# Kernel optimization log

Measured on AMD Instinct MI355X. Metric: run time of the kernel, lower is better.

Reference implementation:

```python
import jax, jax.numpy as jnp
import numpy as np

NUM_HEADS = 16
GROUP_NUM = 4
HIDDEN = 1024
HEAD_DIM = HIDDEN // NUM_HEADS
EPS = 1e-5


def layernorm(x, g, b):
    mu = jnp.mean(x, axis=-1, keepdims=True)
    var = jnp.var(x, axis=-1, keepdims=True)
    return (x - mu) * jax.lax.rsqrt(var + EPS) * g + b


def setup_inputs() -> dict:
    key = jax.random.key(0)
    ks = jax.random.split(key, 12)
    s = 0.02
    return {
        "hidden_state": jax.random.normal(ks[0], (2, 2048, HIDDEN), jnp.float32),
        "wq": jax.random.normal(ks[1], (HIDDEN, HIDDEN), jnp.float32) * s,
        "bq": jnp.zeros((HIDDEN,), jnp.float32),
        "wk": jax.random.normal(ks[2], (GROUP_NUM * HEAD_DIM, HIDDEN), jnp.float32) * s,
        "bk": jnp.zeros((GROUP_NUM * HEAD_DIM,), jnp.float32),
        "wv": jax.random.normal(ks[3], (GROUP_NUM * HEAD_DIM, HIDDEN), jnp.float32) * s,
        "bv": jnp.zeros((GROUP_NUM * HEAD_DIM,), jnp.float32),
        "wo": jax.random.normal(ks[4], (HIDDEN, HIDDEN), jnp.float32) * s,
        "bo": jnp.zeros((HIDDEN,), jnp.float32),
        "ln_g": jnp.ones((HIDDEN,), jnp.float32),
        "ln_b": jnp.zeros((HIDDEN,), jnp.float32),
        "w1": jax.random.normal(ks[5], (HIDDEN, HIDDEN), jnp.float32) * s,
        "b1": jnp.zeros((HIDDEN,), jnp.float32),
        "w2": jax.random.normal(ks[6], (HIDDEN, HIDDEN), jnp.float32) * s,
        "b2": jnp.zeros((HIDDEN,), jnp.float32),
        "fln_g": jnp.ones((HIDDEN,), jnp.float32),
        "fln_b": jnp.zeros((HIDDEN,), jnp.float32),
    }


def reference(hidden_state, wq, bq, wk, bk, wv, bv, wo, bo, ln_g, ln_b,
              w1, b1, w2, b2, fln_g, fln_b):
    B, S, H = hidden_state.shape
    hpg = NUM_HEADS // GROUP_NUM  # heads per KV group

    q = hidden_state @ wq.T + bq  # [B,S,H]
    k = hidden_state @ wk.T + bk  # [B,S,G*D]
    v = hidden_state @ wv.T + bv

    q = q.reshape(B, S, NUM_HEADS, HEAD_DIM).transpose(0, 2, 1, 3)      # [B,Hh,S,D]
    k = k.reshape(B, S, GROUP_NUM, HEAD_DIM).transpose(0, 2, 1, 3)      # [B,G,S,D]
    v = v.reshape(B, S, GROUP_NUM, HEAD_DIM).transpose(0, 2, 1, 3)
    # expand KV groups to full head count (consecutive repeat, matching torch expand+reshape)
    k = jnp.repeat(k, hpg, axis=1)  # [B,Hh,S,D]
    v = jnp.repeat(v, hpg, axis=1)

    scale = 1.0 / jnp.sqrt(jnp.float32(HEAD_DIM))
    scores = jnp.einsum('bhsd,bhtd->bhst', q, k) * scale  # [B,Hh,S,S]
    probs = jax.nn.softmax(scores, axis=-1)
    attn = jnp.einsum('bhst,bhtd->bhsd', probs, v)  # [B,Hh,S,D]

    # Faithful to source: transpose(-1,-2) then raw flat view to [B, S, Hh*D]
    attn = jnp.swapaxes(attn, -1, -2).reshape(B, -1, HEAD_DIM * NUM_HEADS)

    out = layernorm(hidden_state + attn @ wo.T + bo, ln_g, ln_b)
    ffn = out @ w1.T + b1
    ffn = jax.nn.relu(ffn) @ w2.T + b2
    return layernorm(out + ffn, fln_g, fln_b)
```

## Files before the change

### kernel.cpp

```cpp
#include <hip/hip_runtime.h>
#include <math.h>

#define HIDDEN 1024
#define SEQ 2048

typedef __attribute__((ext_vector_type(8))) short short8;
typedef __attribute__((ext_vector_type(4))) float f32x4;

__device__ __forceinline__ unsigned short f2bf(float x) {
  union { float f; unsigned u; } c; c.f = x;
  unsigned r = c.u + 0x7FFFu + ((c.u >> 16) & 1u);
  return (unsigned short)(r >> 16);
}
__device__ __forceinline__ float bf2f(unsigned short h) {
  union { unsigned u; float f; } c; c.u = ((unsigned)h) << 16;
  return c.f;
}

__device__ __forceinline__ float fexp2(float x) {
  float r; asm("v_exp_f32 %0, %1" : "=v"(r) : "v"(x)); return r;
}

__device__ __forceinline__ unsigned cvt_pk_bf16(float lo, float hi) {
  unsigned r;
  asm("v_cvt_pk_bf16_f32 %0, %1, %2" : "=v"(r) : "v"(lo), "v"(hi));
  return r;
}

__device__ __forceinline__ void async_copy16(const void* g, void* l) {
  __builtin_amdgcn_global_load_lds(
      (const __attribute__((address_space(1))) unsigned int*)g,
      (__attribute__((address_space(3))) unsigned int*)l, 16, 0, 0);
}

__global__ __launch_bounds__(256) void cvt_all(
    const float* __restrict__ hs, const float* __restrict__ wq,
    const float* __restrict__ wk, const float* __restrict__ wv,
    const float* __restrict__ wo, const float* __restrict__ w1,
    const float* __restrict__ w2,
    unsigned short* __restrict__ hsb, unsigned short* __restrict__ wqb,
    unsigned short* __restrict__ wkb, unsigned short* __restrict__ wvb,
    unsigned short* __restrict__ wob, unsigned short* __restrict__ w1b,
    unsigned short* __restrict__ w2b)
{
  const int i = blockIdx.x * 256 + threadIdx.x;
  const float* src; unsigned short* dst; int off;
  if (i < 1048576)      { src = hs; dst = hsb; off = i; }
  else if (i < 1310720) { src = wq; dst = wqb; off = i - 1048576; }
  else if (i < 1376256) { src = wk; dst = wkb; off = i - 1310720; }
  else if (i < 1441792) { src = wv; dst = wvb; off = i - 1376256; }
  else if (i < 1703936) { src = wo; dst = wob; off = i - 1441792; }
  else if (i < 1966080) { src = w1; dst = w1b; off = i - 1703936; }
  else                  { src = w2; dst = w2b; off = i - 1966080; }
  float4 v = ((const float4*)src)[off];
  ushort4 o;
  o.x = f2bf(v.x); o.y = f2bf(v.y); o.z = f2bf(v.z); o.w = f2bf(v.w);
  ((ushort4*)dst)[off] = o;
}

template<bool RELU>
__global__ __launch_bounds__(512) void gemm128(
    const unsigned short* __restrict__ A, const unsigned short* __restrict__ W,
    const float* __restrict__ bias, unsigned short* __restrict__ C,
    int M, int N, int K)
{
  __shared__ unsigned short As[2][128 * 64];
  __shared__ unsigned short Bs[2][128 * 64];
  const int tid = threadIdx.x;
  const int lane = tid & 63, wave = tid >> 6;
  const int ln = lane & 15, quad = lane >> 4;
  const int wm = (wave >> 2) * 64, wn = (wave & 3) * 32;

  const int flat = blockIdx.x;
  const int swz = (flat & 7) * ((int)gridDim.x >> 3) + (flat >> 3);
  const int ntx = N >> 7;
  const int m0 = (swz / ntx) * 128, n0 = (swz % ntx) * 128;

  f32x4 acc[4][2];
#pragma unroll
  for (int i = 0; i < 4; ++i)
#pragma unroll
    for (int j = 0; j < 2; ++j) acc[i][j] = (f32x4){0.f, 0.f, 0.f, 0.f};

  auto stage = [&](int k0, int p) {
#pragma unroll
    for (int it = 0; it < 2; ++it) {
      const int c = (wave * 2 + it) * 64 + lane;
      const int row = c >> 3, gc = (c & 7) ^ (row & 7);
      async_copy16(A + (size_t)(m0 + row) * K + k0 + gc * 8,
                   &As[p][(wave * 2 + it) * 512]);
    }
#pragma unroll
    for (int it = 0; it < 2; ++it) {
      const int c = (wave * 2 + it) * 64 + lane;
      const int row = c >> 3, gc = (c & 7) ^ (row & 7);
      async_copy16(W + (size_t)(n0 + row) * K + k0 + gc * 8,
                   &Bs[p][(wave * 2 + it) * 512]);
    }
  };

  stage(0, 0);
  const int NT = K >> 6;
  for (int t = 0; t < NT; ++t) {
    const int p = t & 1;
    if (t < NT - 1) {
      stage((t + 1) * 64, p ^ 1);
      asm volatile("s_waitcnt vmcnt(4)" ::: "memory");
    } else {
      asm volatile("s_waitcnt vmcnt(0)" ::: "memory");
    }
    __builtin_amdgcn_s_barrier();
    asm volatile("" ::: "memory");

    short8 af[4][2], bfr[2][2];
#pragma unroll
    for (int i = 0; i < 4; ++i) {
      const int row = wm + i * 16 + ln;
#pragma unroll
      for (int f = 0; f < 2; ++f) {
        const int ch = row * 8 + ((f * 4 + quad) ^ (row & 7));
        af[i][f] = *(const short8*)&As[p][ch * 8];
      }
    }
#pragma unroll
    for (int j = 0; j < 2; ++j) {
      const int row = wn + j * 16 + ln;
#pragma unroll
      for (int f = 0; f < 2; ++f) {
        const int ch = row * 8 + ((f * 4 + quad) ^ (row & 7));
        bfr[j][f] = *(const short8*)&Bs[p][ch * 8];
      }
    }
#pragma unroll
    for (int i = 0; i < 4; ++i)
#pragma unroll
      for (int j = 0; j < 2; ++j) {
        acc[i][j] = __builtin_amdgcn_mfma_f32_16x16x32_bf16(af[i][0], bfr[j][0], acc[i][j], 0, 0, 0);
        acc[i][j] = __builtin_amdgcn_mfma_f32_16x16x32_bf16(af[i][1], bfr[j][1], acc[i][j], 0, 0, 0);
      }

    asm volatile("" ::: "memory");
    __builtin_amdgcn_s_barrier();
    asm volatile("" ::: "memory");
  }

#pragma unroll
  for (int j = 0; j < 2; ++j) {
    const int n = n0 + wn + j * 16 + ln;
    const float bv = bias[n];
#pragma unroll
    for (int i = 0; i < 4; ++i) {
#pragma unroll
      for (int rr = 0; rr < 4; ++rr) {
        const int m = m0 + wm + i * 16 + quad * 4 + rr;
        float v = acc[i][j][rr] + bv;
        if (RELU) v = fmaxf(v, 0.f);
        C[(size_t)m * N + n] = f2bf(v);
      }
    }
  }
}

__global__ __launch_bounds__(256) void gemm_qkv(
    const unsigned short* __restrict__ A,
    const unsigned short* __restrict__ Wq, const unsigned short* __restrict__ Wk,
    const unsigned short* __restrict__ Wv,
    const float* __restrict__ bq, const float* __restrict__ bk,
    const float* __restrict__ bv,
    unsigned short* __restrict__ Qo, unsigned short* __restrict__ Ko,
    unsigned short* __restrict__ Vt)
{
  __shared__ unsigned short As[64 * 64];
  __shared__ unsigned short Bs[128 * 64];

  const int flat = blockIdx.x;
  const int swz = (flat & 7) * 96 + (flat >> 3);
  const int bx = swz % 12, by = swz / 12;

  int mode, nw0;
  const unsigned short* W;
  const float* bias;
  if (bx < 8)       { mode = 0; W = Wq; bias = bq; nw0 = bx * 128; }
  else if (bx < 10) { mode = 1; W = Wk; bias = bk; nw0 = (bx - 8) * 128; }
  else              { mode = 2; W = Wv; bias = bv; nw0 = (bx - 10) * 128; }

  const int tid = threadIdx.x;
  const int lane = tid & 63, wave = tid >> 6;
  const int ln = lane & 15, quad = lane >> 4;
  const int wm = (wave >> 1) * 32, wn = (wave & 1) * 64;
  const int m0 = by * 64;
  const int K = 1024;

  f32x4 acc[2][4];
#pragma unroll
  for (int i = 0; i < 2; ++i)
#pragma unroll
    for (int j = 0; j < 4; ++j) acc[i][j] = (f32x4){0.f, 0.f, 0.f, 0.f};

  for (int k0 = 0; k0 < K; k0 += 64) {
#pragma unroll
    for (int it = 0; it < 2; ++it) {
      const int c = (wave * 2 + it) * 64 + lane;
      const int row = c >> 3, gc = (c & 7) ^ (row & 7);
      async_copy16(A + (size_t)(m0 + row) * K + k0 + gc * 8,
                   &As[(wave * 2 + it) * 512]);
    }
#pragma unroll
    for (int it = 0; it < 4; ++it) {
      const int c = (wave * 4 + it) * 64 + lane;
      const int row = c >> 3, gc = (c & 7) ^ (row & 7);
      async_copy16(W + (size_t)(nw0 + row) * K + k0 + gc * 8,
                   &Bs[(wave * 4 + it) * 512]);
    }
    __syncthreads();

    short8 af[2][2], bfr[4][2];
#pragma unroll
    for (int i = 0; i < 2; ++i) {
      const int row = wm + i * 16 + ln;
#pragma unroll
      for (int f = 0; f < 2; ++f) {
        const int ch = row * 8 + ((f * 4 + quad) ^ (row & 7));
        af[i][f] = *(const short8*)&As[ch * 8];
      }
    }
#pragma unroll
    for (int j = 0; j < 4; ++j) {
      const int row = wn + j * 16 + ln;
#pragma unroll
      for (int f = 0; f < 2; ++f) {
        const int ch = row * 8 + ((f * 4 + quad) ^ (row & 7));
        bfr[j][f] = *(const short8*)&Bs[ch * 8];
      }
    }
#pragma unroll
    for (int i = 0; i < 2; ++i)
#pragma unroll
      for (int j = 0; j < 4; ++j) {
        acc[i][j] = __builtin_amdgcn_mfma_f32_16x16x32_bf16(af[i][0], bfr[j][0], acc[i][j], 0, 0, 0);
        acc[i][j] = __builtin_amdgcn_mfma_f32_16x16x32_bf16(af[i][1], bfr[j][1], acc[i][j], 0, 0, 0);
      }
    __syncthreads();
  }

#pragma unroll
  for (int j = 0; j < 4; ++j) {
    const int nl = nw0 + wn + j * 16 + ln;
    const float bvv = bias[nl];
#pragma unroll
    for (int i = 0; i < 2; ++i) {
#pragma unroll
      for (int rr = 0; rr < 4; ++rr) {
        const int m = m0 + wm + i * 16 + quad * 4 + rr;
        const float v = acc[i][j][rr] + bvv;
        if (mode == 0) {
          Qo[(size_t)m * 1024 + nl] = f2bf(v);
        } else if (mode == 1) {
          Ko[(size_t)m * 256 + nl] = f2bf(v);
        } else {
          const int b = m >> 11, s = m & 2047;
          Vt[((size_t)b * 256 + nl) * SEQ + s] = f2bf(v);
        }
      }
    }
  }
}

__global__ __launch_bounds__(512, 4) void attn_mfma(
    const unsigned short* __restrict__ Q, const unsigned short* __restrict__ Kb,
    const unsigned short* __restrict__ Vt,
    unsigned short* __restrict__ N0, unsigned short* __restrict__ N1,
    float* __restrict__ LS)
{
  __shared__ unsigned short Ks[2][64 * 64];
  __shared__ unsigned short Vs[2][64 * 64];

  const int hwb = blockIdx.x;
  const int swz = (hwb & 7) * 64 + (hwb >> 3);
  const int qblk = swz & 7, half = (swz >> 3) & 1, h = (swz >> 4) & 15, b = swz >> 8;
  const int g = h >> 2;

  unsigned short* __restrict__ numO = half ? N1 : N0;
  float* __restrict__ lsO = LS + half * 65536;

  const int tid = threadIdx.x, lane = tid & 63, wave = tid >> 6;
  const int ln = lane & 15, quad = lane >> 4, q8 = quad * 8;
  const int s0 = qblk * 256;
  const float qscale = 0.125f * 1.44269504f;

  const int ln7 = ln & 7;
  const int x0 = (quad ^ ln7) * 8;
  const int x1 = ((4 + quad) ^ ln7) * 8;

  short8 ones;
#pragma unroll
  for (int e = 0; e < 8; ++e) ones[e] = (short)0x3F80;

  short8 qf[2][2];
#pragma unroll
  for (int qg = 0; qg < 2; ++qg) {
    const unsigned short* qsrc =
        Q + ((size_t)(b * SEQ + s0 + wave * 32 + qg * 16 + ln)) * 1024 + h * 64 + q8;
    qf[qg][0] = *(const short8*)qsrc;
    qf[qg][1] = *(const short8*)(qsrc + 32);
#pragma unroll
    for (int e = 0; e < 8; ++e) {
      qf[qg][0][e] = (short)f2bf(bf2f((unsigned short)qf[qg][0][e]) * qscale);
      qf[qg][1][e] = (short)f2bf(bf2f((unsigned short)qf[qg][1][e]) * qscale);
    }
  }

  const int srow = lane >> 3;
  const int sgcc = (lane & 7) ^ srow;

  auto stage = [&](int t0, int p) {
    const int row = wave * 8 + srow;
    const int skey = (row & 32) | ((row & 8) << 1) | ((row & 4) << 1) |
                     ((row & 16) >> 2) | (row & 3);
    async_copy16(Kb + (size_t)(b * SEQ + t0 + skey) * 256 + g * 64 + sgcc * 8,
                 &Ks[p][wave * 512]);
    async_copy16(Vt + (size_t)(b * 256 + g * 64 + row) * SEQ + t0 + sgcc * 8,
                 &Vs[p][wave * 512]);
  };

  f32x4 of[2][4];
  f32x4 ls[2];
#pragma unroll
  for (int qg = 0; qg < 2; ++qg) {
    ls[qg] = (f32x4){0.f, 0.f, 0.f, 0.f};
#pragma unroll
    for (int jd = 0; jd < 4; ++jd) of[qg][jd] = (f32x4){0.f, 0.f, 0.f, 0.f};
  }

  const int tbase = half * 16;
  stage(tbase * 64, 0);

  for (int tt = 0; tt < 16; ++tt) {
    const int p = tt & 1;
    if (tt < 15) {
      stage((tbase + tt + 1) * 64, p ^ 1);
      asm volatile("s_waitcnt vmcnt(2)" ::: "memory");
    } else {
      asm volatile("s_waitcnt vmcnt(0)" ::: "memory");
    }
    __builtin_amdgcn_s_barrier();
    asm volatile("" ::: "memory");

    f32x4 sc[2][4];
#pragma unroll
    for (int jn = 0; jn < 4; ++jn) {
      const int krow = (jn * 16 + ln) * 64;
      const short8 kf0 = *(const short8*)&Ks[p][krow + x0];
      const short8 kf1 = *(const short8*)&Ks[p][krow + x1];
#pragma unroll
      for (int qg = 0; qg < 2; ++qg) {
        f32x4 z = (f32x4){0.f, 0.f, 0.f, 0.f};
        z = __builtin_amdgcn_mfma_f32_16x16x32_bf16(kf0, qf[qg][0], z, 0, 0, 0);
        z = __builtin_amdgcn_mfma_f32_16x16x32_bf16(kf1, qf[qg][1], z, 0, 0, 0);
        sc[qg][jn] = z;
      }
    }

    short8 pf[2][2];
#pragma unroll
    for (int qg = 0; qg < 2; ++qg) {
#pragma unroll
      for (int jn = 0; jn < 4; ++jn)
#pragma unroll
        for (int r = 0; r < 4; ++r) sc[qg][jn][r] = fexp2(sc[qg][jn][r]);
#pragma unroll
      for (int F = 0; F < 2; ++F) {
        union { unsigned u[4]; short8 s; } pk;
        pk.u[0] = cvt_pk_bf16(sc[qg][2 * F][0], sc[qg][2 * F][1]);
        pk.u[1] = cvt_pk_bf16(sc[qg][2 * F][2], sc[qg][2 * F][3]);
        pk.u[2] = cvt_pk_bf16(sc[qg][2 * F + 1][0], sc[qg][2 * F + 1][1]);
        pk.u[3] = cvt_pk_bf16(sc[qg][2 * F + 1][2], sc[qg][2 * F + 1][3]);
        pf[qg][F] = pk.s;
      }
      ls[qg] = __builtin_amdgcn_mfma_f32_16x16x32_bf16(pf[qg][0], ones, ls[qg], 0, 0, 0);
      ls[qg] = __builtin_amdgcn_mfma_f32_16x16x32_bf16(pf[qg][1], ones, ls[qg], 0, 0, 0);
    }

#pragma unroll
    for (int jd = 0; jd < 4; ++jd) {
      const int vrow = (jd * 16 + ln) * 64;
      const short8 vf0 = *(const short8*)&Vs[p][vrow + x0];
      const short8 vf1 = *(const short8*)&Vs[p][vrow + x1];
#pragma unroll
      for (int qg = 0; qg < 2; ++qg) {
        of[qg][jd] = __builtin_amdgcn_mfma_f32_16x16x32_bf16(pf[qg][0], vf0, of[qg][jd], 0, 0, 0);
        of[qg][jd] = __builtin_amdgcn_mfma_f32_16x16x32_bf16(pf[qg][1], vf1, of[qg][jd], 0, 0, 0);
      }
    }

    asm volatile("" ::: "memory");
    __builtin_amdgcn_s_barrier();
    asm volatile("" ::: "memory");
  }

#pragma unroll
  for (int qg = 0; qg < 2; ++qg) {
    const int sbase = s0 + wave * 32 + qg * 16 + quad * 4;
    if (ln == 0) {
#pragma unroll
      for (int r = 0; r < 4; ++r)
        lsO[(b * 16 + h) * 2048 + sbase + r] = ls[qg][r];
    }
#pragma unroll
    for (int jd = 0; jd < 4; ++jd) {
      const int d = jd * 16 + ln;
      ushort4 ov;
      ov.x = f2bf(of[qg][jd][0]);
      ov.y = f2bf(of[qg][jd][1]);
      ov.z = f2bf(of[qg][jd][2]);
      ov.w = f2bf(of[qg][jd][3]);
      *(ushort4*)&numO[((size_t)b * 1024 + h * 64 + d) * SEQ + sbase] = ov;
    }
  }
}

__global__ __launch_bounds__(256) void attn_reduce(
    const unsigned short* __restrict__ N0, unsigned short* att,
    const float* __restrict__ LS)
{
  const int i = (blockIdx.x * 256 + threadIdx.x) * 4;
  const int row = i >> 11, s = i & 2047;
  const int h = (row >> 6) & 15, b = row >> 10;
  const int lsi = (b * 16 + h) * 2048 + s;
  const float4 l0 = *(const float4*)&LS[lsi];
  const float4 l1 = *(const float4*)&LS[65536 + lsi];
  const ushort4 a = *(const ushort4*)&N0[i];
  const ushort4 c = *(const ushort4*)&att[i];
  ushort4 o;
  o.x = f2bf((bf2f(a.x) + bf2f(c.x)) / (l0.x + l1.x));
  o.y = f2bf((bf2f(a.y) + bf2f(c.y)) / (l0.y + l1.y));
  o.z = f2bf((bf2f(a.z) + bf2f(c.z)) / (l0.z + l1.z));
  o.w = f2bf((bf2f(a.w) + bf2f(c.w)) / (l0.w + l1.w));
  *(ushort4*)&att[i] = o;
}

__device__ __forceinline__ void ln_core(float x[4], const float* gam, const float* bet,
                                        int tid, float out[4]) {
  float s1 = x[0] + x[1] + x[2] + x[3];
  float s2 = x[0] * x[0] + x[1] * x[1] + x[2] * x[2] + x[3] * x[3];
#pragma unroll
  for (int off = 1; off < 64; off <<= 1) {
    s1 += __shfl_xor(s1, off);
    s2 += __shfl_xor(s2, off);
  }
  __shared__ float r1[4], r2[4];
  const int wave = tid >> 6;
  if ((tid & 63) == 0) { r1[wave] = s1; r2[wave] = s2; }
  __syncthreads();
  s1 = r1[0] + r1[1] + r1[2] + r1[3];
  s2 = r2[0] + r2[1] + r2[2] + r2[3];
  const float mu  = s1 * (1.0f / HIDDEN);
  const float var = s2 * (1.0f / HIDDEN) - mu * mu;
  const float inv = rsqrtf(var + 1e-5f);
  float4 gv = *(const float4*)&gam[tid * 4];
  float4 bv = *(const float4*)&bet[tid * 4];
  out[0] = (x[0] - mu) * inv * gv.x + bv.x;
  out[1] = (x[1] - mu) * inv * gv.y + bv.y;
  out[2] = (x[2] - mu) * inv * gv.z + bv.z;
  out[3] = (x[3] - mu) * inv * gv.w + bv.w;
}

__global__ __launch_bounds__(256) void resid_ln1(
    const float* __restrict__ X, const unsigned short* __restrict__ Y,
    const float* __restrict__ gam, const float* __restrict__ bet,
    unsigned short* __restrict__ outb)
{
  const int row = blockIdx.x, tid = threadIdx.x;
  const size_t base = (size_t)row * HIDDEN + tid * 4;
  float4 a = *(const float4*)&X[base];
  ushort4 yv = *(const ushort4*)&Y[base];
  float x[4] = {a.x + bf2f(yv.x), a.y + bf2f(yv.y), a.z + bf2f(yv.z), a.w + bf2f(yv.w)};
  float o[4];
  ln_core(x, gam, bet, tid, o);
  ushort4 ov;
  ov.x = f2bf(o[0]); ov.y = f2bf(o[1]); ov.z = f2bf(o[2]); ov.w = f2bf(o[3]);
  *(ushort4*)&outb[base] = ov;
}

__global__ __launch_bounds__(256) void resid_ln2(
    const unsigned short* __restrict__ X, const unsigned short* __restrict__ Y,
    const float* __restrict__ gam, const float* __restrict__ bet,
    float* __restrict__ out)
{
  const int row = blockIdx.x, tid = threadIdx.x;
  const size_t base = (size_t)row * HIDDEN + tid * 4;
  ushort4 xv = *(const ushort4*)&X[base];
  ushort4 yv = *(const ushort4*)&Y[base];
  float x[4] = {bf2f(xv.x) + bf2f(yv.x), bf2f(xv.y) + bf2f(yv.y),
                bf2f(xv.z) + bf2f(yv.z), bf2f(xv.w) + bf2f(yv.w)};
  float o[4];
  ln_core(x, gam, bet, tid, o);
  float4 ov; ov.x = o[0]; ov.y = o[1]; ov.z = o[2]; ov.w = o[3];
  *(float4*)&out[base] = ov;
}

extern "C" void kernel_launch(void* const* d_in, const int* in_sizes, int n_in,
                              void* d_out, int out_size, void* d_ws, size_t ws_size,
                              hipStream_t stream)
{
  (void)in_sizes; (void)n_in; (void)out_size; (void)ws_size;
  const float* hs  = (const float*)d_in[0];
  const float* wq  = (const float*)d_in[1];
  const float* bq  = (const float*)d_in[2];
  const float* wk  = (const float*)d_in[3];
  const float* bk  = (const float*)d_in[4];
  const float* wv  = (const float*)d_in[5];
  const float* bvp = (const float*)d_in[6];
  const float* wo  = (const float*)d_in[7];
  const float* bo  = (const float*)d_in[8];
  const float* lng = (const float*)d_in[9];
  const float* lnb = (const float*)d_in[10];
  const float* w1  = (const float*)d_in[11];
  const float* b1  = (const float*)d_in[12];
  const float* w2  = (const float*)d_in[13];
  const float* b2  = (const float*)d_in[14];
  const float* flg = (const float*)d_in[15];
  const float* flb = (const float*)d_in[16];
  float* out = (float*)d_out;

  unsigned short* w = (unsigned short*)d_ws;
  unsigned short* wqb = w;
  unsigned short* wkb = w + 1048576;
  unsigned short* wvb = w + 1310720;
  unsigned short* wob = w + 1572864;
  unsigned short* w1b = w + 2621440;
  unsigned short* w2b = w + 3670016;
  unsigned short* hsb = w + 4718592;
  unsigned short* qb  = w + 8912896;
  unsigned short* kb  = w + 13107200;
  unsigned short* vt  = w + 14155776;
  unsigned short* att = w + 15204352;
  unsigned short* f1b = hsb;
  unsigned short* yb  = qb;
  unsigned short* obb = att;
  unsigned short* f2b = qb;
  float* lsbuf = (float*)wqb;

  dim3 blk(256);
  cvt_all<<<dim3(8704), blk, 0, stream>>>(hs, wq, wk, wv, wo, w1, w2,
                                          hsb, wqb, wkb, wvb, wob, w1b, w2b);

  gemm_qkv<<<dim3(768), blk, 0, stream>>>(hsb, wqb, wkb, wvb, bq, bk, bvp,
                                          qb, kb, vt);
  attn_mfma<<<dim3(512), dim3(512), 0, stream>>>(qb, kb, vt, hsb, att, lsbuf);
  attn_reduce<<<dim3(4096), blk, 0, stream>>>(hsb, att, lsbuf);
  gemm128<false><<<dim3(256), dim3(512), 0, stream>>>(att, wob, bo, yb, 4096, 1024, 1024);
  resid_ln1<<<dim3(4096), blk, 0, stream>>>(hs, yb, lng, lnb, obb);
  gemm128<true><<<dim3(256), dim3(512), 0, stream>>>(obb, w1b, b1, f1b, 4096, 1024, 1024);
  gemm128<false><<<dim3(256), dim3(512), 0, stream>>>(f1b, w2b, b2, f2b, 4096, 1024, 1024);
  resid_ln2<<<dim3(4096), blk, 0, stream>>>(obb, f2b, flg, flb, out);
}
```

Baseline: 236.0 us.

## Replace 128x128 double-buffered GEMM with 64x128 single-buffered 256-thread tiles

The three dense 4096x1024x1024 GEMMs move from a 512-thread 128x128 tile with double-buffered LDS and manual waitcnt pipelining to a 256-thread 64x128 tile with a single LDS buffer and plain __syncthreads. The grid doubles from 256 to 512 blocks, which fills more of the CUs and cuts LDS per block. In exchange it loses the overlap between global loads and MFMA compute, and reuse of each W tile drops because M tiles are smaller.

```diff
diff --git a/kernel.cpp b/kernel.cpp
--- a/kernel.cpp
+++ b/kernel.cpp
@@ -59,97 +59,82 @@
 }
 
 template<bool RELU>
-__global__ __launch_bounds__(512) void gemm128(
+__global__ __launch_bounds__(256) void gemm_wn(
     const unsigned short* __restrict__ A, const unsigned short* __restrict__ W,
     const float* __restrict__ bias, unsigned short* __restrict__ C,
     int M, int N, int K)
 {
-  __shared__ unsigned short As[2][128 * 64];
-  __shared__ unsigned short Bs[2][128 * 64];
+  __shared__ unsigned short As[64 * 64];
+  __shared__ unsigned short Bs[128 * 64];
+
+  const int flat = blockIdx.x;
+  const int swz = (flat & 7) * ((int)gridDim.x >> 3) + (flat >> 3);
+  const int ntx = N >> 7;
+  const int m0 = (swz / ntx) * 64, n0 = (swz % ntx) * 128;
+
   const int tid = threadIdx.x;
   const int lane = tid & 63, wave = tid >> 6;
   const int ln = lane & 15, quad = lane >> 4;
-  const int wm = (wave >> 2) * 64, wn = (wave & 3) * 32;
-
-  const int flat = blockIdx.x;
-  const int swz = (flat & 7) * ((int)gridDim.x >> 3) + (flat >> 3);
-  const int ntx = N >> 7;
-  const int m0 = (swz / ntx) * 128, n0 = (swz % ntx) * 128;
-
-  f32x4 acc[4][2];
-#pragma unroll
-  for (int i = 0; i < 4; ++i)
-#pragma unroll
-    for (int j = 0; j < 2; ++j) acc[i][j] = (f32x4){0.f, 0.f, 0.f, 0.f};
-
-  auto stage = [&](int k0, int p) {
+  const int wm = (wave >> 1) * 32, wn = (wave & 1) * 64;
+
+  f32x4 acc[2][4];
+#pragma unroll
+  for (int i = 0; i < 2; ++i)
+#pragma unroll
+    for (int j = 0; j < 4; ++j) acc[i][j] = (f32x4){0.f, 0.f, 0.f, 0.f};
+
+  for (int k0 = 0; k0 < K; k0 += 64) {
 #pragma unroll
     for (int it = 0; it < 2; ++it) {
       const int c = (wave * 2 + it) * 64 + lane;
       const int row = c >> 3, gc = (c & 7) ^ (row & 7);
       async_copy16(A + (size_t)(m0 + row) * K + k0 + gc * 8,
-                   &As[p][(wave * 2 + it) * 512]);
-    }
-#pragma unroll
-    for (int it = 0; it < 2; ++it) {
-      const int c = (wave * 2 + it) * 64 + lane;
+                   &As[(wave * 2 + it) * 512]);
+    }
+#pragma unroll
+    for (int it = 0; it < 4; ++it) {
+      const int c = (wave * 4 + it) * 64 + lane;
       const int row = c >> 3, gc = (c & 7) ^ (row & 7);
       async_copy16(W + (size_t)(n0 + row) * K + k0 + gc * 8,
-                   &Bs[p][(wave * 2 + it) * 512]);
-    }
-  };
-
-  stage(0, 0);
-  const int NT = K >> 6;
-  for (int t = 0; t < NT; ++t) {
-    const int p = t & 1;
-    if (t < NT - 1) {
-      stage((t + 1) * 64, p ^ 1);
-      asm volatile("s_waitcnt vmcnt(4)" ::: "memory");
-    } else {
-      asm volatile("s_waitcnt vmcnt(0)" ::: "memory");
-    }
-    __builtin_amdgcn_s_barrier();
-    asm volatile("" ::: "memory");
-
-    short8 af[4][2], bfr[2][2];
-#pragma unroll
-    for (int i = 0; i < 4; ++i) {
+                   &Bs[(wave * 4 + it) * 512]);
+    }
+    __syncthreads();
+
+    short8 af[2][2], bfr[4][2];
+#pragma unroll
+    for (int i = 0; i < 2; ++i) {
       const int row = wm + i * 16 + ln;
 #pragma unroll
       for (int f = 0; f < 2; ++f) {
         const int ch = row * 8 + ((f * 4 + quad) ^ (row & 7));
-        af[i][f] = *(const short8*)&As[p][ch * 8];
-      }
-    }
-#pragma unroll
-    for (int j = 0; j < 2; ++j) {
+        af[i][f] = *(const short8*)&As[ch * 8];
+      }
+    }
+#pragma unroll
+    for (int j = 0; j < 4; ++j) {
       const int row = wn + j * 16 + ln;
 #pragma unroll
       for (int f = 0; f < 2; ++f) {
         const int ch = row * 8 + ((f * 4 + quad) ^ (row & 7));
-        bfr[j][f] = *(const short8*)&Bs[p][ch * 8];
-      }
-    }
-#pragma unroll
-    for (int i = 0; i < 4; ++i)
-#pragma unroll
-      for (int j = 0; j < 2; ++j) {
+        bfr[j][f] = *(const short8*)&Bs[ch * 8];
+      }
+    }
+#pragma unroll
+    for (int i = 0; i < 2; ++i)
+#pragma unroll
+      for (int j = 0; j < 4; ++j) {
         acc[i][j] = __builtin_amdgcn_mfma_f32_16x16x32_bf16(af[i][0], bfr[j][0], acc[i][j], 0, 0, 0);
         acc[i][j] = __builtin_amdgcn_mfma_f32_16x16x32_bf16(af[i][1], bfr[j][1], acc[i][j], 0, 0, 0);
       }
-
-    asm volatile("" ::: "memory");
-    __builtin_amdgcn_s_barrier();
-    asm volatile("" ::: "memory");
-  }
-
-#pragma unroll
-  for (int j = 0; j < 2; ++j) {
+    __syncthreads();
+  }
+
+#pragma unroll
+  for (int j = 0; j < 4; ++j) {
     const int n = n0 + wn + j * 16 + ln;
     const float bv = bias[n];
 #pragma unroll
-    for (int i = 0; i < 4; ++i) {
+    for (int i = 0; i < 2; ++i) {
 #pragma unroll
       for (int rr = 0; rr < 4; ++rr) {
         const int m = m0 + wm + i * 16 + quad * 4 + rr;
@@ -549,9 +534,9 @@
                                           qb, kb, vt);
   attn_mfma<<<dim3(512), dim3(512), 0, stream>>>(qb, kb, vt, hsb, att, lsbuf);
   attn_reduce<<<dim3(4096), blk, 0, stream>>>(hsb, att, lsbuf);
-  gemm128<false><<<dim3(256), dim3(512), 0, stream>>>(att, wob, bo, yb, 4096, 1024, 1024);
+  gemm_wn<false><<<dim3(512), blk, 0, stream>>>(att, wob, bo, yb, 4096, 1024, 1024);
   resid_ln1<<<dim3(4096), blk, 0, stream>>>(hs, yb, lng, lnb, obb);
-  gemm128<true><<<dim3(256), dim3(512), 0, stream>>>(obb, w1b, b1, f1b, 4096, 1024, 1024);
-  gemm128<false><<<dim3(256), dim3(512), 0, stream>>>(f1b, w2b, b2, f2b, 4096, 1024, 1024);
+  gemm_wn<true><<<dim3(512), blk, 0, stream>>>(obb, w1b, b1, f1b, 4096, 1024, 1024);
+  gemm_wn<false><<<dim3(512), blk, 0, stream>>>(f1b, w2b, b2, f2b, 4096, 1024, 1024);
   resid_ln2<<<dim3(4096), blk, 0, stream>>>(obb, f2b, flg, flb, out);
 }
```

Result: no change. 234.9 us (-0.4%).
